# Kernel optimization log

Measured on AMD Instinct MI355X. Metric: run time of the kernel, lower is better.

## Reference

```python
import jax, jax.numpy as jnp
import numpy as np

B, C = 65536, 1024

def setup_inputs() -> dict:
    key = jax.random.key(0)
    kx, ky, ku = jax.random.split(key, 3)
    x = jax.random.normal(kx, (B, C), dtype=jnp.float32)
    # binary choice indicator; p small so some rows are all-zero -> exercises both branches
    y = (jax.random.uniform(ky, (B, C)) < 0.003).astype(jnp.float32)
    u = jax.random.normal(ku, (1,), dtype=jnp.float32)  # scalar outside-option utility
    return {"x": x, "y": y, "u": u}

def reference(x, y, u):
    # Original per-row math:
    #   if sum(y_i) > 0: loss_i = log10( exp(sum(x_i*y_i)) / (exp(u) + sum(exp(x_i))) )
    #   else:            loss_i = log10( exp(u)            / (exp(u) + sum(exp(x_i))) )
    # Rewritten stably: log10(exp(s)/(exp(u)+sum exp x)) = (s - logaddexp(u, logsumexp(x))) / ln(10)
    ln10 = jnp.log(jnp.asarray(10.0, dtype=x.dtype))
    u0 = u[0]
    lse = jax.scipy.special.logsumexp(x, axis=1)          # [B]
    log_den = jnp.logaddexp(u0, lse)                      # [B]
    s = jnp.where(jnp.sum(y, axis=1) > 0,
                  jnp.sum(x * y, axis=1),                 # chosen-utility numerator
                  u0)                                     # outside-option numerator
    loss = (s - log_den) / ln10                           # per-row log10 likelihood
    return -jnp.mean(loss)
```

## Files before the change

kernel.cpp:

```cpp
#include <hip/hip_runtime.h>
#include <math.h>

#define B_ROWS 65536
#define C_COLS 1024
#define NBLOCKS 2048
#define WAVES_PER_BLOCK 4
#define NWAVES (NBLOCKS * WAVES_PER_BLOCK)
#define ROWS_PER_WAVE (B_ROWS / NWAVES)

typedef float v4f __attribute__((ext_vector_type(4)));

__global__ __launch_bounds__(256) void mnl_rows_kernel(
    const float* __restrict__ x,
    const float* __restrict__ y,
    const float* __restrict__ u,
    float* __restrict__ partial) {
  const int wave = threadIdx.x >> 6;
  const int lane = threadIdx.x & 63;
  const int gwave = blockIdx.x * WAVES_PER_BLOCK + wave;
  const long long row0 = (long long)gwave * ROWS_PER_WAVE;
  const float u0 = u[0];

  const v4f* __restrict__ xb = (const v4f*)x;
  const v4f* __restrict__ yb = (const v4f*)y;

  float se[ROWS_PER_WAVE], sxy[ROWS_PER_WAVE];
  unsigned choice_mask = 0;

  v4f cx[4], cy[4], nx[4], ny[4];

  {
    const v4f* xr = xb + row0 * (C_COLS / 4) + lane;
    const v4f* yr = yb + row0 * (C_COLS / 4) + lane;
#pragma unroll
    for (int i = 0; i < 4; ++i) {
      cx[i] = __builtin_nontemporal_load(xr + 64 * i);
      cy[i] = __builtin_nontemporal_load(yr + 64 * i);
    }
  }

#pragma unroll
  for (int r = 0; r < ROWS_PER_WAVE; ++r) {
    if (r + 1 < ROWS_PER_WAVE) {
      const v4f* xr = xb + (row0 + r + 1) * (C_COLS / 4) + lane;
      const v4f* yr = yb + (row0 + r + 1) * (C_COLS / 4) + lane;
#pragma unroll
      for (int i = 0; i < 4; ++i) {
        nx[i] = __builtin_nontemporal_load(xr + 64 * i);
        ny[i] = __builtin_nontemporal_load(yr + 64 * i);
      }
    }

    float se_l = 0.f, sxy_l = 0.f, sy_l = 0.f;
#pragma unroll
    for (int i = 0; i < 4; ++i) {
      se_l  += __expf(cx[i].x) + __expf(cx[i].y) +
               __expf(cx[i].z) + __expf(cx[i].w);
      sxy_l += cx[i].x * cy[i].x + cx[i].y * cy[i].y +
               cx[i].z * cy[i].z + cx[i].w * cy[i].w;
      sy_l  += cy[i].x + cy[i].y + cy[i].z + cy[i].w;
    }
    se[r] = se_l;
    sxy[r] = sxy_l;
    choice_mask |= (__any(sy_l > 0.f) ? 1u : 0u) << r;

#pragma unroll
    for (int i = 0; i < 4; ++i) { cx[i] = nx[i]; cy[i] = ny[i]; }
  }

#pragma unroll
  for (int off = 1; off < 64; off <<= 1) {
#pragma unroll
    for (int r = 0; r < ROWS_PER_WAVE; ++r) {
      se[r]  += __shfl_xor(se[r],  off, 64);
      sxy[r] += __shfl_xor(sxy[r], off, 64);
    }
  }

  float acc = 0.f;
#pragma unroll
  for (int r = 0; r < ROWS_PER_WAVE; ++r) {
    const float lse = __logf(se[r]);
    const float a = fmaxf(u0, lse);
    const float logden = a + log1pf(__expf(-fabsf(u0 - lse)));
    const float s = ((choice_mask >> r) & 1u) ? sxy[r] : u0;
    acc += s - logden;
  }

  __shared__ float sh[WAVES_PER_BLOCK];
  if (lane == 0) sh[wave] = acc;
  __syncthreads();
  if (threadIdx.x == 0)
    partial[blockIdx.x] = sh[0] + sh[1] + sh[2] + sh[3];
}

__global__ __launch_bounds__(256) void mnl_reduce_kernel(
    const float* __restrict__ partial, float* __restrict__ out) {
  float acc = 0.f;
  for (int i = threadIdx.x; i < NBLOCKS; i += 256) acc += partial[i];
#pragma unroll
  for (int off = 1; off < 64; off <<= 1) acc += __shfl_xor(acc, off, 64);

  __shared__ float sh[4];
  const int wave = threadIdx.x >> 6;
  const int lane = threadIdx.x & 63;
  if (lane == 0) sh[wave] = acc;
  __syncthreads();
  if (threadIdx.x == 0) {
    const float t = sh[0] + sh[1] + sh[2] + sh[3];
    const float scale = 1.0f / (2.302585092994046f * (float)B_ROWS);
    out[0] = -t * scale;
  }
}

extern "C" void kernel_launch(void* const* d_in, const int* in_sizes, int n_in,
                              void* d_out, int out_size, void* d_ws, size_t ws_size,
                              hipStream_t stream) {
  const float* x = (const float*)d_in[0];
  const float* y = (const float*)d_in[1];
  const float* u = (const float*)d_in[2];
  float* out = (float*)d_out;
  float* partial = (float*)d_ws;

  mnl_rows_kernel<<<NBLOCKS, 256, 0, stream>>>(x, y, u, partial);
  mnl_reduce_kernel<<<1, 256, 0, stream>>>(partial, out);
}
```

Before: 94.28 us.

## Double-buffer half-row loads and double block count with higher occupancy

Doubles the grid to 4096 blocks, so each wave handles 4 rows instead of 8, and adds a launch_bounds occupancy hint of 8 blocks per CU. The prefetch now works on half-row steps with a two-slot ping-pong buffer instead of full-row current/next register sets. This cuts per-thread register use so more waves can be resident to hide memory latency on this bandwidth-bound read of two 256MB arrays. The cost is a larger partial array for the reduce kernel and shallower per-wave prefetch.

```diff
diff --git a/kernel.cpp b/kernel.cpp
--- a/kernel.cpp
+++ b/kernel.cpp
@@ -3,75 +3,72 @@
 
 #define B_ROWS 65536
 #define C_COLS 1024
-#define NBLOCKS 2048
-#define WAVES_PER_BLOCK 4
-#define NWAVES (NBLOCKS * WAVES_PER_BLOCK)
-#define ROWS_PER_WAVE (B_ROWS / NWAVES)
+#define NBLOCKS 4096
+#define WPB 4
+#define NWAVES (NBLOCKS * WPB)
+#define RPW (B_ROWS / NWAVES)
+#define NSTEP (RPW * 2)
 
 typedef float v4f __attribute__((ext_vector_type(4)));
 
-__global__ __launch_bounds__(256) void mnl_rows_kernel(
+__global__ __launch_bounds__(256, 8) void mnl_rows_kernel(
     const float* __restrict__ x,
     const float* __restrict__ y,
     const float* __restrict__ u,
     float* __restrict__ partial) {
   const int wave = threadIdx.x >> 6;
   const int lane = threadIdx.x & 63;
-  const int gwave = blockIdx.x * WAVES_PER_BLOCK + wave;
-  const long long row0 = (long long)gwave * ROWS_PER_WAVE;
+  const int gwave = blockIdx.x * WPB + wave;
+  const long long v0 = (long long)gwave * (RPW * (C_COLS / 4)) + lane;
+  const v4f* __restrict__ xb = (const v4f*)x;
+  const v4f* __restrict__ yb = (const v4f*)y;
   const float u0 = u[0];
 
-  const v4f* __restrict__ xb = (const v4f*)x;
-  const v4f* __restrict__ yb = (const v4f*)y;
-
-  float se[ROWS_PER_WAVE], sxy[ROWS_PER_WAVE];
-  unsigned choice_mask = 0;
-
-  v4f cx[4], cy[4], nx[4], ny[4];
+  v4f bx[2][2], by[2][2];
+  float se[RPW], sxy[RPW];
+  unsigned choice = 0;
 
   {
-    const v4f* xr = xb + row0 * (C_COLS / 4) + lane;
-    const v4f* yr = yb + row0 * (C_COLS / 4) + lane;
-#pragma unroll
-    for (int i = 0; i < 4; ++i) {
-      cx[i] = __builtin_nontemporal_load(xr + 64 * i);
-      cy[i] = __builtin_nontemporal_load(yr + 64 * i);
-    }
+    const v4f* xp = xb + v0;
+    const v4f* yp = yb + v0;
+    bx[0][0] = __builtin_nontemporal_load(xp);
+    bx[0][1] = __builtin_nontemporal_load(xp + 64);
+    by[0][0] = __builtin_nontemporal_load(yp);
+    by[0][1] = __builtin_nontemporal_load(yp + 64);
   }
 
+  float se_l = 0.f, sxy_l = 0.f, sy_l = 0.f;
 #pragma unroll
-  for (int r = 0; r < ROWS_PER_WAVE; ++r) {
-    if (r + 1 < ROWS_PER_WAVE) {
-      const v4f* xr = xb + (row0 + r + 1) * (C_COLS / 4) + lane;
-      const v4f* yr = yb + (row0 + r + 1) * (C_COLS / 4) + lane;
+  for (int s = 0; s < NSTEP; ++s) {
+    if (s + 1 < NSTEP) {
+      const v4f* xp = xb + v0 + (long long)(s + 1) * 128;
+      const v4f* yp = yb + v0 + (long long)(s + 1) * 128;
+      bx[(s + 1) & 1][0] = __builtin_nontemporal_load(xp);
+      bx[(s + 1) & 1][1] = __builtin_nontemporal_load(xp + 64);
+      by[(s + 1) & 1][0] = __builtin_nontemporal_load(yp);
+      by[(s + 1) & 1][1] = __builtin_nontemporal_load(yp + 64);
+    }
 #pragma unroll
-      for (int i = 0; i < 4; ++i) {
-        nx[i] = __builtin_nontemporal_load(xr + 64 * i);
-        ny[i] = __builtin_nontemporal_load(yr + 64 * i);
-      }
+    for (int i = 0; i < 2; ++i) {
+      const v4f xv = bx[s & 1][i];
+      const v4f yv = by[s & 1][i];
+      se_l  += __expf(xv.x) + __expf(xv.y) + __expf(xv.z) + __expf(xv.w);
+      sxy_l += xv.x * yv.x + xv.y * yv.y + xv.z * yv.z + xv.w * yv.w;
+      sy_l  += yv.x + yv.y + yv.z + yv.w;
     }
-
-    float se_l = 0.f, sxy_l = 0.f, sy_l = 0.f;
-#pragma unroll
-    for (int i = 0; i < 4; ++i) {
-      se_l  += __expf(cx[i].x) + __expf(cx[i].y) +
-               __expf(cx[i].z) + __expf(cx[i].w);
-      sxy_l += cx[i].x * cy[i].x + cx[i].y * cy[i].y +
-               cx[i].z * cy[i].z + cx[i].w * cy[i].w;
-      sy_l  += cy[i].x + cy[i].y + cy[i].z + cy[i].w;
+    if (s & 1) {
+      const int r = s >> 1;
+      se[r]  = se_l;
+      sxy[r] = sxy_l;
+      choice |= (__any(sy_l > 0.f) ? 1u : 0u) << r;
+      se_l = 0.f; sxy_l = 0.f; sy_l = 0.f;
     }
-    se[r] = se_l;
-    sxy[r] = sxy_l;
-    choice_mask |= (__any(sy_l > 0.f) ? 1u : 0u) << r;
-
-#pragma unroll
-    for (int i = 0; i < 4; ++i) { cx[i] = nx[i]; cy[i] = ny[i]; }
   }
 
 #pragma unroll
   for (int off = 1; off < 64; off <<= 1) {
 #pragma unroll
-    for (int r = 0; r < ROWS_PER_WAVE; ++r) {
+    for (int r = 0; r < RPW; ++r) {
       se[r]  += __shfl_xor(se[r],  off, 64);
       sxy[r] += __shfl_xor(sxy[r], off, 64);
     }
@@ -79,15 +76,15 @@
 
   float acc = 0.f;
 #pragma unroll
-  for (int r = 0; r < ROWS_PER_WAVE; ++r) {
+  for (int r = 0; r < RPW; ++r) {
     const float lse = __logf(se[r]);
     const float a = fmaxf(u0, lse);
     const float logden = a + log1pf(__expf(-fabsf(u0 - lse)));
-    const float s = ((choice_mask >> r) & 1u) ? sxy[r] : u0;
+    const float s = ((choice >> r) & 1u) ? sxy[r] : u0;
     acc += s - logden;
   }
 
-  __shared__ float sh[WAVES_PER_BLOCK];
+  __shared__ float sh[WPB];
   if (lane == 0) sh[wave] = acc;
   __syncthreads();
   if (threadIdx.x == 0)
```

Measured after the change: 197.6 us. +109.6%, slower.
